# Kernel optimization log

Measured on AMD Instinct MI355X. Metric: run time of the kernel, lower is better.

## Reference

```python
import jax, jax.numpy as jnp
import numpy as np

B, H, HKV, S, D = 1, 32, 4, 2048, 128
NEG = -1e9  # causal mask fill (float32-safe, like torch finfo.min in spirit)


def setup_inputs() -> dict:
    key = jax.random.key(0)
    kq, kk, kv, ks = jax.random.split(key, 4)
    query = jax.random.normal(kq, (B, H, S, D), dtype=jnp.float32)
    k = jax.random.normal(kk, (B, HKV, S, D), dtype=jnp.float32)
    v = jax.random.normal(kv, (B, HKV, S, D), dtype=jnp.float32)
    sinks = jax.random.normal(ks, (H,), dtype=jnp.float32)
    # causal additive mask [B, 1, S, S]
    causal = jnp.where(jnp.tril(jnp.ones((S, S), dtype=bool)), 0.0, NEG).astype(jnp.float32)
    attention_mask = jnp.broadcast_to(causal[None, None], (B, 1, S, S))
    return {"query": query, "key": k, "value": v,
            "attention_mask": attention_mask, "sinks": sinks}


def reference(query, key, value, attention_mask, sinks):
    scaling = 1.0 / jnp.sqrt(jnp.asarray(D, dtype=query.dtype))
    groups = H // HKV
    # repeat_kv: [B, HKV, S, D] -> [B, H, S, D]
    k = jnp.repeat(key, groups, axis=1)
    v = jnp.repeat(value, groups, axis=1)
    # scores [B, H, S, S]
    attn = jnp.einsum('bhqd,bhkd->bhqk', query, k) * scaling
    attn = attn + attention_mask[:, :, :, :attn.shape[-1]]
    # append per-head sink column -> [B, H, S, S+1]
    sink_col = jnp.broadcast_to(sinks.reshape(1, H, 1, 1), (B, H, S, 1)).astype(attn.dtype)
    combined = jnp.concatenate([attn, sink_col], axis=-1)
    combined = combined - jnp.max(combined, axis=-1, keepdims=True)
    probs = jax.nn.softmax(combined, axis=-1)[..., :-1]
    # PV matmul, then [B, H, S, D] -> [B, S, H, D]
    out = jnp.einsum('bhqk,bhkd->bhqd', probs, v)
    return jnp.transpose(out, (0, 2, 1, 3))
```

## Files before the change

kernel.cpp:

```cpp
#include <hip/hip_runtime.h>
#include <hip/hip_bf16.h>


#define NH    32
#define SEQ   2048
#define HD    128
#define KVB   64
#define KTILE 16384
#define KVHB  (32 * KTILE)

typedef __attribute__((ext_vector_type(8)))  short bf16x8;
typedef __attribute__((ext_vector_type(4)))  float f32x4;
typedef __attribute__((ext_vector_type(16))) float f32x16;

#define LGKM0  asm volatile("s_waitcnt lgkmcnt(0)" ::: "memory")
#define VMCNT0 asm volatile("s_waitcnt vmcnt(0)" ::: "memory")

static __device__ __forceinline__ unsigned short f2bf(float f) {
  __hip_bfloat16 h = __float2bfloat16(f);
  union { __hip_bfloat16 h; unsigned short u; } c; c.h = h;
  return c.u;
}
static __device__ __forceinline__ unsigned int pk2(float a, float b) {
  return (unsigned int)f2bf(a) | ((unsigned int)f2bf(b) << 16);
}
static __device__ __forceinline__ bf16x8 mk8(unsigned int w0, unsigned int w1,
                                             unsigned int w2, unsigned int w3) {
  union { unsigned int w[4]; bf16x8 v; } t;
  t.w[0] = w0; t.w[1] = w1; t.w[2] = w2; t.w[3] = w3; return t.v;
}

__global__ __launch_bounds__(256)
void convert_kv(const float* __restrict__ K, const float* __restrict__ V,
                char* __restrict__ Ki, char* __restrict__ Vi)
{
  const int b = blockIdx.x;
  const float* Ks = K + (size_t)b * (KVB * HD);
  const float* Vs = V + (size_t)b * (KVB * HD);
  char* kt = Ki + (size_t)b * KTILE;
  char* vt = Vi + (size_t)b * KTILE;
  const int tid   = threadIdx.x;
  const int r16   = tid >> 4;
  const int dcol  = (tid & 15) * 8;
  const int dstep = dcol >> 4;
  const int h2d   = (dcol >> 3) & 1;
  #pragma unroll
  for (int i = 0; i < 4; ++i) {
    const int row = i * 16 + r16;
    float tk[8], tv[8];
    *(f32x4*)(tk)     = *(const f32x4*)(Ks + row * HD + dcol);
    *(f32x4*)(tk + 4) = *(const f32x4*)(Ks + row * HD + dcol + 4);
    *(f32x4*)(tv)     = *(const f32x4*)(Vs + row * HD + dcol);
    *(f32x4*)(tv + 4) = *(const f32x4*)(Vs + row * HD + dcol + 4);
    bf16x8 k8;
    #pragma unroll
    for (int j = 0; j < 8; ++j) k8[j] = (short)f2bf(tk[j]);
    *(bf16x8*)(kt + ((row >> 5) * 8 + dstep) * 1024 + (h2d * 32 + (row & 31)) * 16) = k8;
    const int s = (row >> 4) & 3, h2v = (row >> 3) & 1, jv = row & 7;
    #pragma unroll
    for (int j = 0; j < 8; ++j) {
      const int d = dcol + j;
      *(unsigned short*)(vt + ((d >> 5) * 4 + s) * 1024 + (h2v * 32 + (d & 31)) * 16 + jv * 2)
        = f2bf(tv[j]);
    }
  }
}

__device__ __forceinline__ void stage2(const char* kimg, const char* vimg,
                                       char* kb, char* vb, int tid) {
  #pragma unroll
  for (int k = 0; k < 4; ++k)
    __builtin_amdgcn_global_load_lds((const unsigned int*)(kimg + k * 4096 + tid * 16),
                                     (unsigned int*)(kb + k * 4096 + tid * 16), 16, 0, 0);
  #pragma unroll
  for (int k = 0; k < 4; ++k)
    __builtin_amdgcn_global_load_lds((const unsigned int*)(vimg + k * 4096 + tid * 16),
                                     (unsigned int*)(vb + k * 4096 + tid * 16), 16, 0, 0);
}

__global__ __launch_bounds__(256, 2)
void attn_fwd(const float* __restrict__ Q, const float* __restrict__ sinks,
              const char* __restrict__ Ki, const char* __restrict__ Vi,
              float* __restrict__ out)
{
  __shared__ __align__(16) char KB[2][16384];
  __shared__ __align__(16) char VB[2][16384];
  __shared__ float sml[2][32];

  const int tid  = threadIdx.x;
  const int lane = tid & 63;
  const int w    = tid >> 6;
  const int qs   = w >> 1;
  const int ws   = w & 1;
  const int lq   = lane & 31;
  const int hi   = lane >> 5;

  const int bid = blockIdx.x;
  const int h   = bid >> 4;
  const int j   = bid & 15;
  const int kvh = h >> 3;

  const char* Kt = Ki + (size_t)kvh * KVHB;
  const char* Vt = Vi + (size_t)kvh * KVHB;

  const float QSC = 0.08838834764831845f * 1.4426950408889634f;
  const float EC  = 17.312340490667562f;
  const float sadd = __builtin_amdgcn_exp2f(sinks[h] * 1.4426950408889634f - EC);

  int cur = 0;
  stage2(Kt, Vt, KB[0], VB[0], tid);

  #pragma unroll 1
  for (int su = 0; su < 2; ++su) {
    const int qt = su ? j : (31 - j);
    const int q0 = qt * 64;
    const int nt = qt + 1;
    const int qb = q0 + qs * 32;
    const int qme = qb + lq;

    bf16x8 qf[8];
    {
      const float* qp = Q + ((size_t)h * SEQ + qme) * HD + hi * 8;
      #pragma unroll
      for (int dstep = 0; dstep < 8; ++dstep) {
        float t0[8];
        *(f32x4*)(t0)     = *(const f32x4*)(qp + dstep * 16);
        *(f32x4*)(t0 + 4) = *(const f32x4*)(qp + dstep * 16 + 4);
        bf16x8 qv;
        #pragma unroll
        for (int jj = 0; jj < 8; ++jj) qv[jj] = (short)f2bf(t0[jj] * QSC);
        qf[dstep] = qv;
      }
    }

    f32x16 acc[4];
    #pragma unroll
    for (int d = 0; d < 4; ++d)
      acc[d] = (f32x16){0.f,0.f,0.f,0.f,0.f,0.f,0.f,0.f,0.f,0.f,0.f,0.f,0.f,0.f,0.f,0.f};
    float lsum = 0.f;

    for (int i = 0; i < nt; ++i) {
      LGKM0; VMCNT0;
      __builtin_amdgcn_s_barrier();
      if (i + 1 < nt)
        stage2(Kt + (size_t)(i + 1) * KTILE,
               Vt + (size_t)(i + 1) * KTILE, KB[cur ^ 1], VB[cur ^ 1], tid);
      else if (su == 0)
        stage2(Kt, Vt, KB[cur ^ 1], VB[cur ^ 1], tid);

      const int kv0 = i * KVB + ws * 32;
      if (kv0 <= qb + 31) {
        const char* kb = KB[cur] + ws * 8192 + lane * 16;
        const char* vb = VB[cur] + lane * 16;

        f32x16 sc = (f32x16){0.f,0.f,0.f,0.f,0.f,0.f,0.f,0.f,0.f,0.f,0.f,0.f,0.f,0.f,0.f,0.f};
        #pragma unroll
        for (int dstep = 0; dstep < 8; ++dstep) {
          bf16x8 kf = *(const bf16x8*)(kb + dstep * 1024);
          sc = __builtin_amdgcn_mfma_f32_32x32x16_bf16(kf, qf[dstep], sc, 0, 0, 0);
        }

        float p[16];
        #pragma unroll
        for (int r = 0; r < 16; ++r)
          p[r] = __builtin_amdgcn_exp2f(sc[r] - EC);
        if (kv0 + 31 > qb) {
          const int kvbase = kv0 + 4 * hi;
          #pragma unroll
          for (int r = 0; r < 16; ++r) {
            const int kv = kvbase + (r & 3) + 8 * (r >> 2);
            if (kv > qme) p[r] = 0.f;
          }
        }
        #pragma unroll
        for (int r = 0; r < 16; ++r) lsum += p[r];

        unsigned int X0 = pk2(p[0],  p[1]),  X1 = pk2(p[2],  p[3]);
        unsigned int Y0 = pk2(p[4],  p[5]),  Y1 = pk2(p[6],  p[7]);
        unsigned int Z0 = pk2(p[8],  p[9]),  Z1 = pk2(p[10], p[11]);
        unsigned int W0 = pk2(p[12], p[13]), W1 = pk2(p[14], p[15]);
        asm volatile("v_permlane32_swap_b32 %0, %1" : "+v"(X0), "+v"(Y0));
        asm volatile("v_permlane32_swap_b32 %0, %1" : "+v"(X1), "+v"(Y1));
        asm volatile("v_permlane32_swap_b32 %0, %1" : "+v"(Z0), "+v"(W0));
        asm volatile("v_permlane32_swap_b32 %0, %1" : "+v"(Z1), "+v"(W1));
        bf16x8 pf0 = mk8(X0, X1, Y0, Y1);
        bf16x8 pf1 = mk8(Z0, Z1, W0, W1);

        #pragma unroll
        for (int dblk = 0; dblk < 4; ++dblk) {
          bf16x8 vf0 = *(const bf16x8*)(vb + (dblk * 4 + ws * 2 + 0) * 1024);
          bf16x8 vf1 = *(const bf16x8*)(vb + (dblk * 4 + ws * 2 + 1) * 1024);
          acc[dblk] = __builtin_amdgcn_mfma_f32_32x32x16_bf16(vf0, pf0, acc[dblk], 0, 0, 0);
          acc[dblk] = __builtin_amdgcn_mfma_f32_32x32x16_bf16(vf1, pf1, acc[dblk], 0, 0, 0);
        }
      }
      cur ^= 1;
    }

    lsum += __shfl_xor(lsum, 32);
    char* scratch = (qs == 0) ? KB[cur ^ 1] : VB[cur ^ 1];
    LGKM0; VMCNT0;
    __builtin_amdgcn_s_barrier();
    if (ws == 1) {
      #pragma unroll
      for (int dblk = 0; dblk < 4; ++dblk)
        #pragma unroll
        for (int m = 0; m < 4; ++m) {
          f32x4 t;
          #pragma unroll
          for (int e = 0; e < 4; ++e) t[e] = acc[dblk][4 * m + e];
          *(f32x4*)(scratch + lq * 512 +
                    ((dblk * 128 + m * 32 + hi * 16) ^ ((lq & 7) << 4))) = t;
        }
      if (lane < 32) sml[qs][lq] = lsum;
    }
    LGKM0;
    __builtin_amdgcn_s_barrier();
    if (ws == 0) {
      #pragma unroll
      for (int dblk = 0; dblk < 4; ++dblk)
        #pragma unroll
        for (int m = 0; m < 4; ++m) {
          f32x4 t = *(const f32x4*)(scratch + lq * 512 +
                     ((dblk * 128 + m * 32 + hi * 16) ^ ((lq & 7) << 4)));
          #pragma unroll
          for (int e = 0; e < 4; ++e) acc[dblk][4 * m + e] += t[e];
        }
      LGKM0;
      const float rd = 1.0f / (lsum + sml[qs][lq] + sadd);

      const int qrow = lane >> 1;
      const int half = lane & 1;
      const int sx   = qrow & 7;
      #pragma unroll
      for (int dblk = 0; dblk < 4; ++dblk) {
        #pragma unroll
        for (int m = 0; m < 4; ++m) {
          f32x4 t;
          #pragma unroll
          for (int e = 0; e < 4; ++e) t[e] = acc[dblk][4 * m + e] * rd;
          *(f32x4*)(scratch + lq * 128 + ((m * 32 + hi * 16) ^ ((lq & 7) << 4))) = t;
        }
        LGKM0;
        float* og = out + (((size_t)(qb + qrow)) * NH + h) * HD + dblk * 32 + half * 16;
        #pragma unroll
        for (int c = 0; c < 4; ++c) {
          f32x4 t = *(const f32x4*)(scratch + qrow * 128 + (((half * 4 + c) ^ sx) * 16));
          *(f32x4*)(og + c * 4) = t;
        }
        LGKM0;
      }
    }
  }
}

extern "C" void kernel_launch(void* const* d_in, const int* in_sizes, int n_in,
                              void* d_out, int out_size, void* d_ws, size_t ws_size,
                              hipStream_t stream) {
  const float* Q     = (const float*)d_in[0];
  const float* K     = (const float*)d_in[1];
  const float* V     = (const float*)d_in[2];
  const float* sinks = (const float*)d_in[4];
  float* out = (float*)d_out;

  char* Ki = (char*)d_ws;
  char* Vi = Ki + (size_t)4 * KVHB;

  convert_kv<<<dim3(128), 256, 0, stream>>>(K, V, Ki, Vi);
  attn_fwd<<<dim3(512), 256, 0, stream>>>(Q, sinks, Ki, Vi, out);
}
```

Baseline: 75.43 us.

## Software-pipeline QK and softmax/PV stages across KV tiles with triple-buffered V

Restructures the KV loop so the QK^T MFMA for tile i is issued before the softmax and PV MFMAs of tile i-1, using two score registers and a triple-buffered V tile in LDS. The goal is to overlap exp/pack work with matrix ops and hide LDS latency. It also drops the cross-segment prefetch of tile 0, which is now reloaded at the start of each segment, and adds an end-of-segment barrier. LDS use grows by one 16KB V buffer, which may reduce occupancy below 2 blocks per CU, and the extra score registers add register pressure.

```diff
diff --git a/kernel.cpp b/kernel.cpp
--- a/kernel.cpp
+++ b/kernel.cpp
@@ -1,6 +1,5 @@
 #include <hip/hip_runtime.h>
 #include <hip/hip_bf16.h>
-
 
 #define NH    32
 #define SEQ   2048
@@ -84,8 +83,7 @@
               float* __restrict__ out)
 {
   __shared__ __align__(16) char KB[2][16384];
-  __shared__ __align__(16) char VB[2][16384];
-  __shared__ float sml[2][32];
+  __shared__ __align__(16) char VB[3][16384];
 
   const int tid  = threadIdx.x;
   const int lane = tid & 63;
@@ -107,9 +105,6 @@
   const float EC  = 17.312340490667562f;
   const float sadd = __builtin_amdgcn_exp2f(sinks[h] * 1.4426950408889634f - EC);
 
-  int cur = 0;
-  stage2(Kt, Vt, KB[0], VB[0], tid);
-
   #pragma unroll 1
   for (int su = 0; su < 2; ++su) {
     const int qt = su ? j : (31 - j);
@@ -118,6 +113,8 @@
     const int qb = q0 + qs * 32;
     const int qme = qb + lq;
 
+    stage2(Kt, Vt, KB[0], VB[0], tid);
+
     bf16x8 qf[8];
     {
       const float* qp = Q + ((size_t)h * SEQ + qme) * HD + hi * 8;
@@ -138,67 +135,81 @@
     for (int d = 0; d < 4; ++d)
       acc[d] = (f32x16){0.f,0.f,0.f,0.f,0.f,0.f,0.f,0.f,0.f,0.f,0.f,0.f,0.f,0.f,0.f,0.f};
     float lsum = 0.f;
-
-    for (int i = 0; i < nt; ++i) {
-      LGKM0; VMCNT0;
+    f32x16 scA, scB;
+
+    auto smpv = [&](int t, const f32x16& S) {
+      const int kv0 = t * KVB + ws * 32;
+      if (kv0 > qb + 31) return;
+      float p[16];
+      #pragma unroll
+      for (int r = 0; r < 16; ++r)
+        p[r] = __builtin_amdgcn_exp2f(S[r] - EC);
+      if (kv0 + 31 > qb) {
+        const int kvbase = kv0 + 4 * hi;
+        #pragma unroll
+        for (int r = 0; r < 16; ++r) {
+          const int kv = kvbase + (r & 3) + 8 * (r >> 2);
+          if (kv > qme) p[r] = 0.f;
+        }
+      }
+      #pragma unroll
+      for (int r = 0; r < 16; ++r) lsum += p[r];
+
+      unsigned int X0 = pk2(p[0],  p[1]),  X1 = pk2(p[2],  p[3]);
+      unsigned int Y0 = pk2(p[4],  p[5]),  Y1 = pk2(p[6],  p[7]);
+      unsigned int Z0 = pk2(p[8],  p[9]),  Z1 = pk2(p[10], p[11]);
+      unsigned int W0 = pk2(p[12], p[13]), W1 = pk2(p[14], p[15]);
+      asm volatile("v_permlane32_swap_b32 %0, %1" : "+v"(X0), "+v"(Y0));
+      asm volatile("v_permlane32_swap_b32 %0, %1" : "+v"(X1), "+v"(Y1));
+      asm volatile("v_permlane32_swap_b32 %0, %1" : "+v"(Z0), "+v"(W0));
+      asm volatile("v_permlane32_swap_b32 %0, %1" : "+v"(Z1), "+v"(W1));
+      bf16x8 pf0 = mk8(X0, X1, Y0, Y1);
+      bf16x8 pf1 = mk8(Z0, Z1, W0, W1);
+
+      const char* vb = VB[t % 3] + lane * 16;
+      #pragma unroll
+      for (int dblk = 0; dblk < 4; ++dblk) {
+        bf16x8 vf0 = *(const bf16x8*)(vb + (dblk * 4 + ws * 2 + 0) * 1024);
+        bf16x8 vf1 = *(const bf16x8*)(vb + (dblk * 4 + ws * 2 + 1) * 1024);
+        acc[dblk] = __builtin_amdgcn_mfma_f32_32x32x16_bf16(vf0, pf0, acc[dblk], 0, 0, 0);
+        acc[dblk] = __builtin_amdgcn_mfma_f32_32x32x16_bf16(vf1, pf1, acc[dblk], 0, 0, 0);
+      }
+    };
+
+    auto ival = [&](int i, f32x16& SCN) {
+      VMCNT0;
       __builtin_amdgcn_s_barrier();
       if (i + 1 < nt)
-        stage2(Kt + (size_t)(i + 1) * KTILE,
-               Vt + (size_t)(i + 1) * KTILE, KB[cur ^ 1], VB[cur ^ 1], tid);
-      else if (su == 0)
-        stage2(Kt, Vt, KB[cur ^ 1], VB[cur ^ 1], tid);
-
+        stage2(Kt + (size_t)(i + 1) * KTILE, Vt + (size_t)(i + 1) * KTILE,
+               KB[(i + 1) & 1], VB[(i + 1) % 3], tid);
       const int kv0 = i * KVB + ws * 32;
       if (kv0 <= qb + 31) {
-        const char* kb = KB[cur] + ws * 8192 + lane * 16;
-        const char* vb = VB[cur] + lane * 16;
-
-        f32x16 sc = (f32x16){0.f,0.f,0.f,0.f,0.f,0.f,0.f,0.f,0.f,0.f,0.f,0.f,0.f,0.f,0.f,0.f};
+        const char* kb = KB[i & 1] + ws * 8192 + lane * 16;
+        f32x16 s = (f32x16){0.f,0.f,0.f,0.f,0.f,0.f,0.f,0.f,
+                            0.f,0.f,0.f,0.f,0.f,0.f,0.f,0.f};
         #pragma unroll
         for (int dstep = 0; dstep < 8; ++dstep) {
           bf16x8 kf = *(const bf16x8*)(kb + dstep * 1024);
-          sc = __builtin_amdgcn_mfma_f32_32x32x16_bf16(kf, qf[dstep], sc, 0, 0, 0);
-        }
-
-        float p[16];
-        #pragma unroll
-        for (int r = 0; r < 16; ++r)
-          p[r] = __builtin_amdgcn_exp2f(sc[r] - EC);
-        if (kv0 + 31 > qb) {
-          const int kvbase = kv0 + 4 * hi;
-          #pragma unroll
-          for (int r = 0; r < 16; ++r) {
-            const int kv = kvbase + (r & 3) + 8 * (r >> 2);
-            if (kv > qme) p[r] = 0.f;
-          }
-        }
-        #pragma unroll
-        for (int r = 0; r < 16; ++r) lsum += p[r];
-
-        unsigned int X0 = pk2(p[0],  p[1]),  X1 = pk2(p[2],  p[3]);
-        unsigned int Y0 = pk2(p[4],  p[5]),  Y1 = pk2(p[6],  p[7]);
-        unsigned int Z0 = pk2(p[8],  p[9]),  Z1 = pk2(p[10], p[11]);
-        unsigned int W0 = pk2(p[12], p[13]), W1 = pk2(p[14], p[15]);
-        asm volatile("v_permlane32_swap_b32 %0, %1" : "+v"(X0), "+v"(Y0));
-        asm volatile("v_permlane32_swap_b32 %0, %1" : "+v"(X1), "+v"(Y1));
-        asm volatile("v_permlane32_swap_b32 %0, %1" : "+v"(Z0), "+v"(W0));
-        asm volatile("v_permlane32_swap_b32 %0, %1" : "+v"(Z1), "+v"(W1));
-        bf16x8 pf0 = mk8(X0, X1, Y0, Y1);
-        bf16x8 pf1 = mk8(Z0, Z1, W0, W1);
-
-        #pragma unroll
-        for (int dblk = 0; dblk < 4; ++dblk) {
-          bf16x8 vf0 = *(const bf16x8*)(vb + (dblk * 4 + ws * 2 + 0) * 1024);
-          bf16x8 vf1 = *(const bf16x8*)(vb + (dblk * 4 + ws * 2 + 1) * 1024);
-          acc[dblk] = __builtin_amdgcn_mfma_f32_32x32x16_bf16(vf0, pf0, acc[dblk], 0, 0, 0);
-          acc[dblk] = __builtin_amdgcn_mfma_f32_32x32x16_bf16(vf1, pf1, acc[dblk], 0, 0, 0);
-        }
-      }
-      cur ^= 1;
-    }
+          s = __builtin_amdgcn_mfma_f32_32x32x16_bf16(kf, qf[dstep], s, 0, 0, 0);
+        }
+        SCN = s;
+      }
+    };
+
+    int i = 0;
+    for (;;) {
+      ival(i, scA);
+      if (i >= 1) smpv(i - 1, scB);
+      ++i; if (i >= nt) break;
+      ival(i, scB);
+      smpv(i - 1, scA);
+      ++i; if (i >= nt) break;
+    }
+    if ((nt - 1) & 1) smpv(nt - 1, scB); else smpv(nt - 1, scA);
 
     lsum += __shfl_xor(lsum, 32);
-    char* scratch = (qs == 0) ? KB[cur ^ 1] : VB[cur ^ 1];
+    char* scratch = KB[qs];
+    float* smlp = (float*)(&VB[0][0]) + qs * 32;
     LGKM0; VMCNT0;
     __builtin_amdgcn_s_barrier();
     if (ws == 1) {
@@ -212,7 +223,7 @@
           *(f32x4*)(scratch + lq * 512 +
                     ((dblk * 128 + m * 32 + hi * 16) ^ ((lq & 7) << 4))) = t;
         }
-      if (lane < 32) sml[qs][lq] = lsum;
+      if (lane < 32) smlp[lq] = lsum;
     }
     LGKM0;
     __builtin_amdgcn_s_barrier();
@@ -227,7 +238,7 @@
           for (int e = 0; e < 4; ++e) acc[dblk][4 * m + e] += t[e];
         }
       LGKM0;
-      const float rd = 1.0f / (lsum + sml[qs][lq] + sadd);
+      const float rd = 1.0f / (lsum + smlp[lq] + sadd);
 
       const int qrow = lane >> 1;
       const int half = lane & 1;
@@ -251,6 +262,8 @@
         LGKM0;
       }
     }
+    LGKM0; VMCNT0;
+    __builtin_amdgcn_s_barrier();
   }
 }
 
```

After: 80.20 us. 1.06x slower.

## Software-pipeline QK and PV MFMAs across tiles with triple-buffered V

Applied to the files above, without the earlier changes.

Restructures the KV loop so the PV matmul for tile i-1 is issued after the QK matmul of tile i, overlapping the exp/pack softmax work with MFMA execution. V tiles are now triple-buffered in LDS so tile i-1's V stays valid while tile i+1 is prefetched, and s_setprio raises wave priority around MFMA bursts. The sum scratch moves into a free K buffer to offset the extra LDS. This costs more LDS per block, which may reduce occupancy below two blocks per CU, and adds register pressure from the extra P fragments.

```diff
diff --git a/kernel.cpp b/kernel.cpp
--- a/kernel.cpp
+++ b/kernel.cpp
@@ -1,6 +1,5 @@
 #include <hip/hip_runtime.h>
 #include <hip/hip_bf16.h>
-
 
 #define NH    32
 #define SEQ   2048
@@ -84,8 +83,7 @@
               float* __restrict__ out)
 {
   __shared__ __align__(16) char KB[2][16384];
-  __shared__ __align__(16) char VB[2][16384];
-  __shared__ float sml[2][32];
+  __shared__ __align__(16) char VB[3][16384];
 
   const int tid  = threadIdx.x;
   const int lane = tid & 63;
@@ -107,9 +105,9 @@
   const float EC  = 17.312340490667562f;
   const float sadd = __builtin_amdgcn_exp2f(sinks[h] * 1.4426950408889634f - EC);
 
-  int cur = 0;
   stage2(Kt, Vt, KB[0], VB[0], tid);
 
+  int gbase = 0;
   #pragma unroll 1
   for (int su = 0; su < 2; ++su) {
     const int qt = su ? j : (31 - j);
@@ -138,28 +136,53 @@
     for (int d = 0; d < 4; ++d)
       acc[d] = (f32x16){0.f,0.f,0.f,0.f,0.f,0.f,0.f,0.f,0.f,0.f,0.f,0.f,0.f,0.f,0.f,0.f};
     float lsum = 0.f;
-
-    for (int i = 0; i < nt; ++i) {
-      LGKM0; VMCNT0;
+    bf16x8 pfA0, pfA1, pfB0, pfB1;
+
+    auto pv = [&](int t, bf16x8& i0, bf16x8& i1) {
+      const int kvp = t * KVB + ws * 32;
+      if (kvp > qb + 31) return;
+      const char* vb = VB[(gbase + t) % 3] + lane * 16;
+      __builtin_amdgcn_s_setprio(1);
+      #pragma unroll
+      for (int dblk = 0; dblk < 4; ++dblk) {
+        bf16x8 vf0 = *(const bf16x8*)(vb + (dblk * 4 + ws * 2 + 0) * 1024);
+        bf16x8 vf1 = *(const bf16x8*)(vb + (dblk * 4 + ws * 2 + 1) * 1024);
+        acc[dblk] = __builtin_amdgcn_mfma_f32_32x32x16_bf16(vf0, i0, acc[dblk], 0, 0, 0);
+        acc[dblk] = __builtin_amdgcn_mfma_f32_32x32x16_bf16(vf1, i1, acc[dblk], 0, 0, 0);
+      }
+      __builtin_amdgcn_s_setprio(0);
+    };
+
+    auto step = [&](int I, bf16x8& o0, bf16x8& o1, bf16x8& i0, bf16x8& i1, bool dopv) {
+      const int g = gbase + I;
+      VMCNT0;
       __builtin_amdgcn_s_barrier();
-      if (i + 1 < nt)
-        stage2(Kt + (size_t)(i + 1) * KTILE,
-               Vt + (size_t)(i + 1) * KTILE, KB[cur ^ 1], VB[cur ^ 1], tid);
+      if (I + 1 < nt)
+        stage2(Kt + (size_t)(I + 1) * KTILE, Vt + (size_t)(I + 1) * KTILE,
+               KB[(g + 1) & 1], VB[(g + 1) % 3], tid);
       else if (su == 0)
-        stage2(Kt, Vt, KB[cur ^ 1], VB[cur ^ 1], tid);
-
-      const int kv0 = i * KVB + ws * 32;
-      if (kv0 <= qb + 31) {
-        const char* kb = KB[cur] + ws * 8192 + lane * 16;
-        const char* vb = VB[cur] + lane * 16;
-
-        f32x16 sc = (f32x16){0.f,0.f,0.f,0.f,0.f,0.f,0.f,0.f,0.f,0.f,0.f,0.f,0.f,0.f,0.f,0.f};
+        stage2(Kt, Vt, KB[(g + 1) & 1], VB[(g + 1) % 3], tid);
+
+      const int kv0 = I * KVB + ws * 32;
+      const bool act = (kv0 <= qb + 31);
+      f32x16 sc;
+      if (act) {
+        const char* kb = KB[g & 1] + ws * 8192 + lane * 16;
+        f32x16 s = (f32x16){0.f,0.f,0.f,0.f,0.f,0.f,0.f,0.f,
+                            0.f,0.f,0.f,0.f,0.f,0.f,0.f,0.f};
+        __builtin_amdgcn_s_setprio(1);
         #pragma unroll
         for (int dstep = 0; dstep < 8; ++dstep) {
           bf16x8 kf = *(const bf16x8*)(kb + dstep * 1024);
-          sc = __builtin_amdgcn_mfma_f32_32x32x16_bf16(kf, qf[dstep], sc, 0, 0, 0);
-        }
-
+          s = __builtin_amdgcn_mfma_f32_32x32x16_bf16(kf, qf[dstep], s, 0, 0, 0);
+        }
+        __builtin_amdgcn_s_setprio(0);
+        sc = s;
+      }
+
+      if (dopv) pv(I - 1, i0, i1);
+
+      if (act) {
         float p[16];
         #pragma unroll
         for (int r = 0; r < 16; ++r)
@@ -174,7 +197,6 @@
         }
         #pragma unroll
         for (int r = 0; r < 16; ++r) lsum += p[r];
-
         unsigned int X0 = pk2(p[0],  p[1]),  X1 = pk2(p[2],  p[3]);
         unsigned int Y0 = pk2(p[4],  p[5]),  Y1 = pk2(p[6],  p[7]);
         unsigned int Z0 = pk2(p[8],  p[9]),  Z1 = pk2(p[10], p[11]);
@@ -183,22 +205,28 @@
         asm volatile("v_permlane32_swap_b32 %0, %1" : "+v"(X1), "+v"(Y1));
         asm volatile("v_permlane32_swap_b32 %0, %1" : "+v"(Z0), "+v"(W0));
         asm volatile("v_permlane32_swap_b32 %0, %1" : "+v"(Z1), "+v"(W1));
-        bf16x8 pf0 = mk8(X0, X1, Y0, Y1);
-        bf16x8 pf1 = mk8(Z0, Z1, W0, W1);
-
-        #pragma unroll
-        for (int dblk = 0; dblk < 4; ++dblk) {
-          bf16x8 vf0 = *(const bf16x8*)(vb + (dblk * 4 + ws * 2 + 0) * 1024);
-          bf16x8 vf1 = *(const bf16x8*)(vb + (dblk * 4 + ws * 2 + 1) * 1024);
-          acc[dblk] = __builtin_amdgcn_mfma_f32_32x32x16_bf16(vf0, pf0, acc[dblk], 0, 0, 0);
-          acc[dblk] = __builtin_amdgcn_mfma_f32_32x32x16_bf16(vf1, pf1, acc[dblk], 0, 0, 0);
-        }
-      }
-      cur ^= 1;
-    }
-
+        o0 = mk8(X0, X1, Y0, Y1);
+        o1 = mk8(Z0, Z1, W0, W1);
+      }
+    };
+
+    step(0, pfA0, pfA1, pfB0, pfB1, false);
+    {
+      int i = 1;
+      for (;;) {
+        if (i >= nt) break;
+        step(i, pfB0, pfB1, pfA0, pfA1, true); ++i;
+        if (i >= nt) break;
+        step(i, pfA0, pfA1, pfB0, pfB1, true); ++i;
+      }
+    }
+    if (nt & 1) pv(nt - 1, pfA0, pfA1);
+    else        pv(nt - 1, pfB0, pfB1);
+
+    const int gnext = gbase + nt;
+    char* scratch = (char*)VB[(gnext % 3 + 1 + qs) % 3];
+    float* smlp = (float*)(KB[(gnext & 1) ^ 1]);
     lsum += __shfl_xor(lsum, 32);
-    char* scratch = (qs == 0) ? KB[cur ^ 1] : VB[cur ^ 1];
     LGKM0; VMCNT0;
     __builtin_amdgcn_s_barrier();
     if (ws == 1) {
@@ -212,7 +240,7 @@
           *(f32x4*)(scratch + lq * 512 +
                     ((dblk * 128 + m * 32 + hi * 16) ^ ((lq & 7) << 4))) = t;
         }
-      if (lane < 32) sml[qs][lq] = lsum;
+      if (lane < 32) smlp[qs * 32 + lq] = lsum;
     }
     LGKM0;
     __builtin_amdgcn_s_barrier();
@@ -227,7 +255,7 @@
           for (int e = 0; e < 4; ++e) acc[dblk][4 * m + e] += t[e];
         }
       LGKM0;
-      const float rd = 1.0f / (lsum + sml[qs][lq] + sadd);
+      const float rd = 1.0f / (lsum + smlp[qs * 32 + lq] + sadd);
 
       const int qrow = lane >> 1;
       const int half = lane & 1;
@@ -251,6 +279,7 @@
         LGKM0;
       }
     }
+    gbase = gnext;
   }
 }
 
```

Result: no change. 74.44 us (-1.3%).

## Split KV tile prefetch into four phased chunks interleaved with compute stages

Applied to the files above, without the earlier changes.

Each KV iteration now has four barrier-separated phases. Every phase issues a quarter of the next tile's global-to-LDS loads and runs part of the QK or PV MFMAs, with partial vmcnt waits in place of full drains. The loads run as one continuous stream across both q-tiles through a global counter. The change also adds s_setprio around the MFMA blocks. The aim is to overlap load latency with compute and avoid the full vmcnt(0) stall every iteration, at the cost of more barriers per tile and tighter vmcnt accounting.

```diff
diff --git a/kernel.cpp b/kernel.cpp
--- a/kernel.cpp
+++ b/kernel.cpp
@@ -1,6 +1,5 @@
 #include <hip/hip_runtime.h>
 #include <hip/hip_bf16.h>
-
 
 #define NH    32
 #define SEQ   2048
@@ -14,7 +13,9 @@
 typedef __attribute__((ext_vector_type(16))) float f32x16;
 
 #define LGKM0  asm volatile("s_waitcnt lgkmcnt(0)" ::: "memory")
-#define VMCNT0 asm volatile("s_waitcnt vmcnt(0)" ::: "memory")
+#define VMW4   asm volatile("s_waitcnt vmcnt(4)" ::: "memory")
+#define VMW6   asm volatile("s_waitcnt vmcnt(6)" ::: "memory")
+#define BAR()  __builtin_amdgcn_s_barrier()
 
 static __device__ __forceinline__ unsigned short f2bf(float f) {
   __hip_bfloat16 h = __float2bfloat16(f);
@@ -66,16 +67,9 @@
   }
 }
 
-__device__ __forceinline__ void stage2(const char* kimg, const char* vimg,
-                                       char* kb, char* vb, int tid) {
-  #pragma unroll
-  for (int k = 0; k < 4; ++k)
-    __builtin_amdgcn_global_load_lds((const unsigned int*)(kimg + k * 4096 + tid * 16),
-                                     (unsigned int*)(kb + k * 4096 + tid * 16), 16, 0, 0);
-  #pragma unroll
-  for (int k = 0; k < 4; ++k)
-    __builtin_amdgcn_global_load_lds((const unsigned int*)(vimg + k * 4096 + tid * 16),
-                                     (unsigned int*)(vb + k * 4096 + tid * 16), 16, 0, 0);
+static __device__ __forceinline__ void sload(const char* img, char* buf, int q, int tid) {
+  __builtin_amdgcn_global_load_lds((const unsigned int*)(img + q * 4096 + tid * 16),
+                                   (unsigned int*)(buf + q * 4096 + tid * 16), 16, 0, 0);
 }
 
 __global__ __launch_bounds__(256, 2)
@@ -99,6 +93,8 @@
   const int h   = bid >> 4;
   const int j   = bid & 15;
   const int kvh = h >> 3;
+  const int nt0 = 32 - j;
+  const int ntot = 33;
 
   const char* Kt = Ki + (size_t)kvh * KVHB;
   const char* Vt = Vi + (size_t)kvh * KVHB;
@@ -107,9 +103,12 @@
   const float EC  = 17.312340490667562f;
   const float sadd = __builtin_amdgcn_exp2f(sinks[h] * 1.4426950408889634f - EC);
 
-  int cur = 0;
-  stage2(Kt, Vt, KB[0], VB[0], tid);
-
+  #pragma unroll
+  for (int q = 0; q < 4; ++q) sload(Kt, KB[0], q, tid);
+  #pragma unroll
+  for (int q = 0; q < 4; ++q) sload(Vt, VB[0], q, tid);
+
+  int g = 0;
   #pragma unroll 1
   for (int su = 0; su < 2; ++su) {
     const int qt = su ? j : (31 - j);
@@ -139,27 +138,49 @@
       acc[d] = (f32x16){0.f,0.f,0.f,0.f,0.f,0.f,0.f,0.f,0.f,0.f,0.f,0.f,0.f,0.f,0.f,0.f};
     float lsum = 0.f;
 
-    for (int i = 0; i < nt; ++i) {
-      LGKM0; VMCNT0;
-      __builtin_amdgcn_s_barrier();
-      if (i + 1 < nt)
-        stage2(Kt + (size_t)(i + 1) * KTILE,
-               Vt + (size_t)(i + 1) * KTILE, KB[cur ^ 1], VB[cur ^ 1], tid);
-      else if (su == 0)
-        stage2(Kt, Vt, KB[cur ^ 1], VB[cur ^ 1], tid);
-
+    for (int i = 0; i < nt; ++i, ++g) {
+      const int gp = g & 1, gn = gp ^ 1;
+      const bool dn = (g + 1 < ntot);
+      const int srcn = (g + 1 < nt0) ? (g + 1) : (g + 1 - nt0);
+      const char* Kn = Kt + (size_t)srcn * KTILE;
+      const char* Vn = Vt + (size_t)srcn * KTILE;
       const int kv0 = i * KVB + ws * 32;
-      if (kv0 <= qb + 31) {
-        const char* kb = KB[cur] + ws * 8192 + lane * 16;
-        const char* vb = VB[cur] + lane * 16;
-
-        f32x16 sc = (f32x16){0.f,0.f,0.f,0.f,0.f,0.f,0.f,0.f,0.f,0.f,0.f,0.f,0.f,0.f,0.f,0.f};
-        #pragma unroll
-        for (int dstep = 0; dstep < 8; ++dstep) {
+      const bool act = (kv0 <= qb + 31);
+      const char* kb = KB[gp] + ws * 8192 + lane * 16;
+      const char* vb = VB[gp] + lane * 16;
+      f32x16 sc;
+      bf16x8 pf0, pf1;
+
+      VMW4; BAR();
+      if (dn) { sload(Kn, KB[gn], 0, tid); sload(Kn, KB[gn], 1, tid); }
+      if (act) {
+        f32x16 s = (f32x16){0.f,0.f,0.f,0.f,0.f,0.f,0.f,0.f,
+                            0.f,0.f,0.f,0.f,0.f,0.f,0.f,0.f};
+        __builtin_amdgcn_s_setprio(1);
+        #pragma unroll
+        for (int dstep = 0; dstep < 4; ++dstep) {
+          bf16x8 kf = *(const bf16x8*)(kb + dstep * 1024);
+          s = __builtin_amdgcn_mfma_f32_32x32x16_bf16(kf, qf[dstep], s, 0, 0, 0);
+        }
+        __builtin_amdgcn_s_setprio(0);
+        sc = s;
+      }
+
+      BAR();
+      if (dn) { sload(Kn, KB[gn], 2, tid); sload(Kn, KB[gn], 3, tid); }
+      if (act) {
+        __builtin_amdgcn_s_setprio(1);
+        #pragma unroll
+        for (int dstep = 4; dstep < 8; ++dstep) {
           bf16x8 kf = *(const bf16x8*)(kb + dstep * 1024);
           sc = __builtin_amdgcn_mfma_f32_32x32x16_bf16(kf, qf[dstep], sc, 0, 0, 0);
         }
-
+        __builtin_amdgcn_s_setprio(0);
+      }
+
+      VMW6; BAR();
+      if (dn) { sload(Vn, VB[gn], 0, tid); sload(Vn, VB[gn], 1, tid); }
+      if (act) {
         float p[16];
         #pragma unroll
         for (int r = 0; r < 16; ++r)
@@ -174,7 +195,6 @@
         }
         #pragma unroll
         for (int r = 0; r < 16; ++r) lsum += p[r];
-
         unsigned int X0 = pk2(p[0],  p[1]),  X1 = pk2(p[2],  p[3]);
         unsigned int Y0 = pk2(p[4],  p[5]),  Y1 = pk2(p[6],  p[7]);
         unsigned int Z0 = pk2(p[8],  p[9]),  Z1 = pk2(p[10], p[11]);
@@ -183,24 +203,39 @@
         asm volatile("v_permlane32_swap_b32 %0, %1" : "+v"(X1), "+v"(Y1));
         asm volatile("v_permlane32_swap_b32 %0, %1" : "+v"(Z0), "+v"(W0));
         asm volatile("v_permlane32_swap_b32 %0, %1" : "+v"(Z1), "+v"(W1));
-        bf16x8 pf0 = mk8(X0, X1, Y0, Y1);
-        bf16x8 pf1 = mk8(Z0, Z1, W0, W1);
-
-        #pragma unroll
-        for (int dblk = 0; dblk < 4; ++dblk) {
+        pf0 = mk8(X0, X1, Y0, Y1);
+        pf1 = mk8(Z0, Z1, W0, W1);
+        __builtin_amdgcn_s_setprio(1);
+        #pragma unroll
+        for (int dblk = 0; dblk < 2; ++dblk) {
           bf16x8 vf0 = *(const bf16x8*)(vb + (dblk * 4 + ws * 2 + 0) * 1024);
           bf16x8 vf1 = *(const bf16x8*)(vb + (dblk * 4 + ws * 2 + 1) * 1024);
           acc[dblk] = __builtin_amdgcn_mfma_f32_32x32x16_bf16(vf0, pf0, acc[dblk], 0, 0, 0);
           acc[dblk] = __builtin_amdgcn_mfma_f32_32x32x16_bf16(vf1, pf1, acc[dblk], 0, 0, 0);
         }
-      }
-      cur ^= 1;
-    }
-
+        __builtin_amdgcn_s_setprio(0);
+      }
+
+      VMW6; BAR();
+      if (dn) { sload(Vn, VB[gn], 2, tid); sload(Vn, VB[gn], 3, tid); }
+      if (act) {
+        __builtin_amdgcn_s_setprio(1);
+        #pragma unroll
+        for (int dblk = 2; dblk < 4; ++dblk) {
+          bf16x8 vf0 = *(const bf16x8*)(vb + (dblk * 4 + ws * 2 + 0) * 1024);
+          bf16x8 vf1 = *(const bf16x8*)(vb + (dblk * 4 + ws * 2 + 1) * 1024);
+          acc[dblk] = __builtin_amdgcn_mfma_f32_32x32x16_bf16(vf0, pf0, acc[dblk], 0, 0, 0);
+          acc[dblk] = __builtin_amdgcn_mfma_f32_32x32x16_bf16(vf1, pf1, acc[dblk], 0, 0, 0);
+        }
+        __builtin_amdgcn_s_setprio(0);
+      }
+    }
+
+    const int dead = (g & 1) ^ 1;
+    char* scratch = qs ? (char*)VB[dead] : (char*)KB[dead];
     lsum += __shfl_xor(lsum, 32);
-    char* scratch = (qs == 0) ? KB[cur ^ 1] : VB[cur ^ 1];
-    LGKM0; VMCNT0;
-    __builtin_amdgcn_s_barrier();
+    LGKM0;
+    BAR();
     if (ws == 1) {
       #pragma unroll
       for (int dblk = 0; dblk < 4; ++dblk)
@@ -215,7 +250,7 @@
       if (lane < 32) sml[qs][lq] = lsum;
     }
     LGKM0;
-    __builtin_amdgcn_s_barrier();
+    BAR();
     if (ws == 0) {
       #pragma unroll
       for (int dblk = 0; dblk < 4; ++dblk)
@@ -251,6 +286,7 @@
         LGKM0;
       }
     }
+    BAR();
   }
 }
 
```

New measurement: 89.64 us. 18.8% more time.
